# Optimization experiments

Hardware: AMD Instinct MI355X
Metric: run time of the kernel (lower is better)

Reference implementation:

```python
import jax, jax.numpy as jnp
import numpy as np

B, S, D = 2, 2048, 1024
N_HEADS = 16
HEAD_DIM = D // N_HEADS  # 64, even for RoPE
THETA = 10000.0


def rope_tables(seq, head_dim, dtype=jnp.float32):
    half = head_dim // 2
    freqs = 1.0 / (THETA ** (jnp.arange(half, dtype=jnp.float32) / half))
    angles = jnp.arange(seq, dtype=jnp.float32)[:, None] * freqs[None, :]  # [S, half]
    return jnp.cos(angles).astype(dtype), jnp.sin(angles).astype(dtype)


def apply_rope_interleaved(x, cos, sin):
    # x: [b, h, s, d]; even/odd interleaving
    x_even = x[..., 0::2]
    x_odd = x[..., 1::2]
    r_even = x_even * cos - x_odd * sin
    r_odd = x_even * sin + x_odd * cos
    # interleave back: stack on last axis then reshape
    out = jnp.stack([r_even, r_odd], axis=-1).reshape(x.shape)
    return out


def setup_inputs() -> dict:
    key = jax.random.key(0)
    ks = jax.random.split(key, 6)
    scale = 1.0 / np.sqrt(D)
    return {
        "x": jax.random.normal(ks[0], (B, S, D), dtype=jnp.float32),
        "Wq": jax.random.normal(ks[1], (D, D), dtype=jnp.float32) * scale,
        "Wk": jax.random.normal(ks[2], (D, D), dtype=jnp.float32) * scale,
        "Wv": jax.random.normal(ks[3], (D, D), dtype=jnp.float32) * scale,
        "Wo": jax.random.normal(ks[4], (D, D), dtype=jnp.float32) * scale,
        "bo": jnp.zeros((D,), dtype=jnp.float32),
    }


def reference(x, Wq, Wk, Wv, Wo, bo):
    b, s, _ = x.shape
    # QKV projections (no bias), split heads -> [b, h, s, hd]
    def proj(W):
        return jnp.einsum('bsd,de->bse', x, W).reshape(b, s, N_HEADS, HEAD_DIM).transpose(0, 2, 1, 3)
    q, k, v = proj(Wq), proj(Wk), proj(Wv)

    cos, sin = rope_tables(s, HEAD_DIM, x.dtype)  # [s, hd//2]
    q = apply_rope_interleaved(q, cos, sin)
    k = apply_rope_interleaved(k, cos, sin)

    scale = 1.0 / jnp.sqrt(jnp.asarray(HEAD_DIM, dtype=x.dtype))
    scores = jnp.einsum('bhqd,bhkd->bhqk', q, k) * scale  # [b, h, s, s]
    causal = jnp.tril(jnp.ones((s, s), dtype=bool))
    scores = jnp.where(causal[None, None], scores, jnp.asarray(-jnp.inf, dtype=scores.dtype))
    attn = jax.nn.softmax(scores, axis=-1)
    ctx = jnp.einsum('bhqk,bhkd->bhqd', attn, v)  # [b, h, s, hd]
    ctx = ctx.transpose(0, 2, 1, 3).reshape(b, s, N_HEADS * HEAD_DIM)
    return jnp.einsum('bsd,de->bse', ctx, Wo) + bo
```

## Files before the change

### kernel.cpp

```cpp
#include <hip/hip_runtime.h>
#include <hip/hip_bf16.h>
#include <math.h>

constexpr int Bb   = 2;
constexpr int S    = 2048;
constexpr int D    = 1024;
constexpr int H    = 16;
constexpr int Dh   = 64;
constexpr int HALF = 32;
constexpr int M    = Bb * S;
constexpr int K    = 1024;
constexpr int N    = 1024;

typedef __attribute__((ext_vector_type(8))) short short8;
typedef __attribute__((ext_vector_type(4))) float f32x4;

__device__ __forceinline__ unsigned short f2bf(float f) {
    unsigned int u = __float_as_uint(f);
    unsigned int r = (u + 0x7fffu + ((u >> 16) & 1u)) >> 16;
    return (unsigned short)r;
}

__device__ __forceinline__ void gl_lds16(const unsigned short* g, unsigned short* lds_base) {
    __builtin_amdgcn_global_load_lds(
        (const __attribute__((address_space(1))) unsigned int*)g,
        (__attribute__((address_space(3))) unsigned int*)lds_base, 16, 0, 0);
}

__global__ __launch_bounds__(256) void prep_kernel(
    const float* __restrict__ x,
    const float* W0, const float* W1, const float* W2, const float* W3,
    unsigned short* __restrict__ xb,
    unsigned short* T0, unsigned short* T1, unsigned short* T2, unsigned short* T3,
    float* __restrict__ cosT, float* __restrict__ sinT)
{
    __shared__ float tile[64][65];
    const int bid = blockIdx.x;
    const int tid = threadIdx.x;

    if (bid < 256) {
        int idx = bid * 256 + tid;
        int s = idx >> 5;
        int i = idx & 31;
        double freq = exp(-(double)i * (log(10000.0) / 32.0));
        double ang  = (double)s * freq;
        cosT[idx] = (float)cos(ang);
        sinT[idx] = (float)sin(ang);
    } else if (bid < 256 + 4096) {
        size_t i = (size_t)(bid - 256) * 256 + tid;
        float4 v = *(const float4*)(x + i * 4);
        ushort4 pk;
        pk.x = f2bf(v.x); pk.y = f2bf(v.y); pk.z = f2bf(v.z); pk.w = f2bf(v.w);
        *(ushort4*)(xb + i * 4) = pk;
    } else {
        int wb = bid - 4352;
        int z  = wb >> 8;
        int rem = wb & 255;
        const float* W = (z == 0) ? W0 : (z == 1) ? W1 : (z == 2) ? W2 : W3;
        unsigned short* T = (z == 0) ? T0 : (z == 1) ? T1 : (z == 2) ? T2 : T3;
        const int bk = (rem >> 4) * 64;
        const int bn = (rem & 15) * 64;
        const int lr = tid >> 4;
        const int lc = (tid & 15) * 4;

        #pragma unroll
        for (int i = 0; i < 4; ++i) {
            int r = lr + i * 16;
            float4 v = *(const float4*)(W + (size_t)(bk + r) * N + bn + lc);
            tile[r][lc + 0] = v.x; tile[r][lc + 1] = v.y;
            tile[r][lc + 2] = v.z; tile[r][lc + 3] = v.w;
        }
        __syncthreads();
        #pragma unroll
        for (int i = 0; i < 4; ++i) {
            int nr = lr + i * 16;
            ushort4 pk;
            pk.x = f2bf(tile[lc + 0][nr]);
            pk.y = f2bf(tile[lc + 1][nr]);
            pk.z = f2bf(tile[lc + 2][nr]);
            pk.w = f2bf(tile[lc + 3][nr]);
            *(ushort4*)(T + (size_t)(bn + nr) * K + bk + lc) = pk;
        }
    }
}

__global__ __launch_bounds__(512, 2) void gemm_qkv_kernel(
    const unsigned short* __restrict__ A,
    const unsigned short* __restrict__ BT,
    unsigned short* outQ, unsigned short* outK, unsigned short* outV,
    const float* __restrict__ cosT, const float* __restrict__ sinT)
{
    constexpr int NT    = 16;
    constexpr int ASLOT = 256 * 64;
    constexpr int BSLOT = 192 * 64;
    __shared__ __align__(16) unsigned short As[2 * ASLOT];
    __shared__ __align__(16) unsigned short Bs[2 * BSLOT];

    const int tid  = threadIdx.x;
    const int wid  = tid >> 6;
    const int lane = tid & 63;
    const int col  = lane & 15;
    const int quad = lane >> 4;
    const int wr   = wid >> 2;
    const int wc   = wid & 3;

    const int mbase = blockIdx.y * 256;
    const int nbase = blockIdx.x * 192;

    const int srow8 = lane >> 3;
    const int sch8  = lane & 7;
    const unsigned short *pA[4], *pB[3];
    unsigned short *dA[4], *dB[3];
    #pragma unroll
    for (int w = 0; w < 4; ++w) {
        int r = wid * 32 + w * 8 + srow8;
        pA[w] = A + (size_t)(mbase + r) * K + ((sch8 + (r >> 1)) & 7) * 8;
        dA[w] = &As[(wid * 32 + w * 8) * 64];
    }
    #pragma unroll
    for (int w = 0; w < 3; ++w) {
        int r = wid * 24 + w * 8 + srow8;
        pB[w] = BT + (size_t)(nbase + r) * K + ((sch8 + (r >> 1)) & 7) * 8;
        dB[w] = &Bs[(wid * 24 + w * 8) * 64];
    }

    int aoff[2][8], boff[2][3];
    #pragma unroll
    for (int kh = 0; kh < 2; ++kh) {
        #pragma unroll
        for (int f = 0; f < 8; ++f) {
            int r = wr * 128 + f * 16 + col;
            aoff[kh][f] = r * 64 + (((kh * 4 + quad) - (r >> 1)) & 7) * 8;
        }
        #pragma unroll
        for (int n = 0; n < 3; ++n) {
            int r = wc * 48 + n * 16 + col;
            boff[kh][n] = r * 64 + (((kh * 4 + quad) - (r >> 1)) & 7) * 8;
        }
    }

    f32x4 acc[8][3];
    #pragma unroll
    for (int f = 0; f < 8; ++f)
        #pragma unroll
        for (int n = 0; n < 3; ++n) acc[f][n] = (f32x4)0.f;

    auto stageA = [&](int slot) {
        #pragma unroll
        for (int w = 0; w < 4; ++w) { gl_lds16(pA[w], dA[w] + slot * ASLOT); pA[w] += 64; }
    };
    auto stageB = [&](int slot) {
        #pragma unroll
        for (int w = 0; w < 3; ++w) { gl_lds16(pB[w], dB[w] + slot * BSLOT); pB[w] += 64; }
    };

    stageA(0); stageB(0);
    asm volatile("s_waitcnt vmcnt(0)" ::: "memory");
    __builtin_amdgcn_s_barrier();
    __builtin_amdgcn_sched_barrier(0);

    #pragma unroll 1
    for (int t = 0; t < NT; ++t) {
        const unsigned short* Ab = &As[(t & 1) * ASLOT];
        const unsigned short* Bc = &Bs[(t & 1) * BSLOT];
        const int ns = (t + 1) & 1;
        short8 af[4], bf[3];

        #pragma unroll
        for (int i = 0; i < 4; ++i) af[i] = *(const short8*)&Ab[aoff[0][i]];
        #pragma unroll
        for (int n = 0; n < 3; ++n) bf[n] = *(const short8*)&Bc[boff[0][n]];
        if (t < NT - 1) stageA(ns);
        __builtin_amdgcn_sched_barrier(0);
        __builtin_amdgcn_s_barrier();
        asm volatile("s_waitcnt lgkmcnt(0)" ::: "memory");
        __builtin_amdgcn_s_setprio(1);
        #pragma unroll
        for (int i = 0; i < 4; ++i)
            #pragma unroll
            for (int n = 0; n < 3; ++n)
                acc[i][n] = __builtin_amdgcn_mfma_f32_16x16x32_bf16(af[i], bf[n], acc[i][n], 0, 0, 0);
        __builtin_amdgcn_s_setprio(0);
        __builtin_amdgcn_sched_barrier(0);
        __builtin_amdgcn_s_barrier();
        __builtin_amdgcn_sched_barrier(0);

        #pragma unroll
        for (int i = 0; i < 4; ++i) af[i] = *(const short8*)&Ab[aoff[0][4 + i]];
        if (t < NT - 1) stageB(ns);
        __builtin_amdgcn_sched_barrier(0);
        __builtin_amdgcn_s_barrier();
        asm volatile("s_waitcnt lgkmcnt(0)" ::: "memory");
        __builtin_amdgcn_s_setprio(1);
        #pragma unroll
        for (int i = 0; i < 4; ++i)
            #pragma unroll
            for (int n = 0; n < 3; ++n)
                acc[4 + i][n] = __builtin_amdgcn_mfma_f32_16x16x32_bf16(af[i], bf[n], acc[4 + i][n], 0, 0, 0);
        __builtin_amdgcn_s_setprio(0);
        __builtin_amdgcn_sched_barrier(0);
        __builtin_amdgcn_s_barrier();
        __builtin_amdgcn_sched_barrier(0);

        #pragma unroll
        for (int i = 0; i < 4; ++i) af[i] = *(const short8*)&Ab[aoff[1][i]];
        #pragma unroll
        for (int n = 0; n < 3; ++n) bf[n] = *(const short8*)&Bc[boff[1][n]];
        __builtin_amdgcn_sched_barrier(0);
        __builtin_amdgcn_s_barrier();
        asm volatile("s_waitcnt lgkmcnt(0)" ::: "memory");
        __builtin_amdgcn_s_setprio(1);
        #pragma unroll
        for (int i = 0; i < 4; ++i)
            #pragma unroll
            for (int n = 0; n < 3; ++n)
                acc[i][n] = __builtin_amdgcn_mfma_f32_16x16x32_bf16(af[i], bf[n], acc[i][n], 0, 0, 0);
        __builtin_amdgcn_s_setprio(0);
        __builtin_amdgcn_sched_barrier(0);
        __builtin_amdgcn_s_barrier();
        __builtin_amdgcn_sched_barrier(0);

        #pragma unroll
        for (int i = 0; i < 4; ++i) af[i] = *(const short8*)&Ab[aoff[1][4 + i]];
        __builtin_amdgcn_sched_barrier(0);
        __builtin_amdgcn_s_barrier();
        asm volatile("s_waitcnt lgkmcnt(0)" ::: "memory");
        __builtin_amdgcn_s_setprio(1);
        #pragma unroll
        for (int i = 0; i < 4; ++i)
            #pragma unroll
            for (int n = 0; n < 3; ++n)
                acc[4 + i][n] = __builtin_amdgcn_mfma_f32_16x16x32_bf16(af[i], bf[n], acc[4 + i][n], 0, 0, 0);
        __builtin_amdgcn_s_setprio(0);
        if (t < NT - 1) { asm volatile("s_waitcnt vmcnt(0)" ::: "memory"); }
        __builtin_amdgcn_sched_barrier(0);
        __builtin_amdgcn_s_barrier();
        __builtin_amdgcn_sched_barrier(0);
    }

    #pragma unroll
    for (int n = 0; n < 3; ++n) {
        int n_g = nbase + wc * 48 + n * 16 + col;
        int z   = n_g >> 10;
        int nl  = n_g & 1023;
        int h = nl >> 6, dh0 = nl & 63;
        if (z < 2) {
            unsigned short* o = z ? outK : outQ;
            int p = dh0 >> 1;
            bool even = !(dh0 & 1);
            #pragma unroll
            for (int f = 0; f < 8; ++f)
                #pragma unroll
                for (int reg = 0; reg < 4; ++reg) {
                    int m_g = mbase + wr * 128 + f * 16 + quad * 4 + reg;
                    int b = m_g >> 11, s = m_g & 2047;
                    float v = acc[f][n][reg];
                    float part = __shfl_xor(v, 1, 64);
                    float c = cosT[s * HALF + p], sn = sinT[s * HALF + p];
                    float r = even ? (v * c - part * sn) : (v * c + part * sn);
                    o[((size_t)(b * H + h) * S + s) * Dh + dh0] = f2bf(r);
                }
        } else {
            #pragma unroll
            for (int f = 0; f < 8; ++f) {
                int m0 = mbase + wr * 128 + f * 16 + quad * 4;
                int b = m0 >> 11, s = m0 & 2047;
                ushort4 pk;
                pk.x = f2bf(acc[f][n][0]);
                pk.y = f2bf(acc[f][n][1]);
                pk.z = f2bf(acc[f][n][2]);
                pk.w = f2bf(acc[f][n][3]);
                *(ushort4*)&outV[((size_t)(b * H + h) * Dh + dh0) * S + s] = pk;
            }
        }
    }
}

__global__ __launch_bounds__(256) void gemm_out_kernel(
    const unsigned short* __restrict__ A,
    const unsigned short* __restrict__ BT,
    float* __restrict__ outO, const float* __restrict__ bias)
{
    constexpr int BK   = 64;
    constexpr int ABUF = 64 * BK;
    constexpr int BBUF = 64 * BK;
    __shared__ __align__(16) unsigned short As[2 * ABUF];
    __shared__ __align__(16) unsigned short Bs[2 * BBUF];

    const int tid  = threadIdx.x;
    const int wave = tid >> 6;
    const int lane = tid & 63;
    const int col  = lane & 15;
    const int quad = lane >> 4;
    const int wy   = wave >> 1;
    const int wx   = wave & 1;

    const int mbase = blockIdx.y * 64;
    const int nbase = blockIdx.x * 64;

    const int srow8 = lane >> 3;
    const int sch8  = lane & 7;

    const unsigned short *pA[2], *pB[2];
    unsigned short *dA[2], *dB[2];
    #pragma unroll
    for (int w = 0; w < 2; ++w) {
        int base = wave * 16 + w * 8;
        int tr = base + srow8;
        pA[w] = A  + (size_t)(mbase + tr) * K + ((sch8 + (tr >> 1)) & 7) * 8;
        pB[w] = BT + (size_t)(nbase + tr) * K + ((sch8 + (tr >> 1)) & 7) * 8;
        dA[w] = &As[base * BK];
        dB[w] = &Bs[base * BK];
    }

    int aoff[2][2], boff[2][2];
    #pragma unroll
    for (int ks = 0; ks < 2; ++ks) {
        #pragma unroll
        for (int mi = 0; mi < 2; ++mi) {
            int r = wy * 32 + mi * 16 + col;
            aoff[ks][mi] = r * BK + (((ks * 4 + quad) - (r >> 1)) & 7) * 8;
        }
        #pragma unroll
        for (int ni = 0; ni < 2; ++ni) {
            int r = wx * 32 + ni * 16 + col;
            boff[ks][ni] = r * BK + (((ks * 4 + quad) - (r >> 1)) & 7) * 8;
        }
    }

    f32x4 acc[2][2];
    #pragma unroll
    for (int mi = 0; mi < 2; ++mi)
        #pragma unroll
        for (int ni = 0; ni < 2; ++ni) acc[mi][ni] = (f32x4)0.f;

    auto stage = [&](int buf) {
        #pragma unroll
        for (int w = 0; w < 2; ++w) { gl_lds16(pA[w], dA[w] + buf * ABUF); pA[w] += BK; }
        #pragma unroll
        for (int w = 0; w < 2; ++w) { gl_lds16(pB[w], dB[w] + buf * BBUF); pB[w] += BK; }
    };
    auto compute = [&](int buf) {
        const unsigned short* Ac = &As[buf * ABUF];
        const unsigned short* Bc = &Bs[buf * BBUF];
        #pragma unroll
        for (int ks = 0; ks < 2; ++ks) {
            short8 af[2], bfr[2];
            #pragma unroll
            for (int mi = 0; mi < 2; ++mi) af[mi] = *(const short8*)&Ac[aoff[ks][mi]];
            #pragma unroll
            for (int ni = 0; ni < 2; ++ni) bfr[ni] = *(const short8*)&Bc[boff[ks][ni]];
            #pragma unroll
            for (int mi = 0; mi < 2; ++mi)
                #pragma unroll
                for (int ni = 0; ni < 2; ++ni)
                    acc[mi][ni] = __builtin_amdgcn_mfma_f32_16x16x32_bf16(af[mi], bfr[ni], acc[mi][ni], 0, 0, 0);
        }
    };

    stage(0);
    #pragma unroll 1
    for (int kk = 0; kk < 16; kk += 2) {
        __syncthreads();
        if (kk + 1 < 16) stage(1);
        compute(0);
        __syncthreads();
        if (kk + 2 < 16) stage(0);
        compute(1);
    }

    #pragma unroll
    for (int ni = 0; ni < 2; ++ni) {
        int n_g = nbase + wx * 32 + ni * 16 + col;
        float bv = bias[n_g];
        #pragma unroll
        for (int mi = 0; mi < 2; ++mi)
            #pragma unroll
            for (int reg = 0; reg < 4; ++reg) {
                int m_g = mbase + wy * 32 + mi * 16 + quad * 4 + reg;
                outO[(size_t)m_g * N + n_g] = acc[mi][ni][reg] + bv;
            }
    }
}

__global__ __launch_bounds__(256) void attn_mfma_kernel(
    const unsigned short* __restrict__ q, const unsigned short* __restrict__ k,
    const unsigned short* __restrict__ vt,
    float* __restrict__ Opart, float* __restrict__ lpart)
{
    constexpr int TSZ = 64 * 64;
    __shared__ __align__(16) unsigned short Ks[2 * TSZ];
    __shared__ __align__(16) unsigned short Vs[2 * TSZ];
    __shared__ __align__(16) unsigned short Ps[4][16 * 64];

    const int tid  = threadIdx.x;
    const int wave = tid >> 6;
    const int lane = tid & 63;
    const int col  = lane & 15;
    const int quad = lane >> 4;
    const int l8   = lane >> 3, cp = lane & 7;

    const int pairh = blockIdx.x;
    const int pair  = pairh >> 1;
    const int hpar  = pairh & 1;
    const int bh = blockIdx.y;
    const unsigned short* qb = q  + (size_t)bh * S * Dh;
    const unsigned short* kb = k  + (size_t)bh * S * Dh;
    const unsigned short* vb = vt + (size_t)bh * Dh * S;

    unsigned short* dk0 = &Ks[(wave * 16 + 0) * 64];
    unsigned short* dk1 = &Ks[(wave * 16 + 8) * 64];
    unsigned short* dv0 = &Vs[(wave * 16 + 0) * 64];
    unsigned short* dv1 = &Vs[(wave * 16 + 8) * 64];

    int foff[2][4];
    #pragma unroll
    for (int ks = 0; ks < 2; ++ks)
        #pragma unroll
        for (int nt = 0; nt < 4; ++nt) {
            int r = nt * 16 + col;
            foff[ks][nt] = r * 64 + (((ks * 4 + quad) - r) & 7) * 8;
        }
    int poffW[4][4];
    #pragma unroll
    for (int nt = 0; nt < 4; ++nt)
        #pragma unroll
        for (int reg = 0; reg < 4; ++reg) {
            int row = quad * 4 + reg;
            poffW[nt][reg] = row * 64 + (((nt * 2 + (col >> 3)) ^ (row & 7)) << 3) + (col & 7);
        }
    int poffR[2];
    #pragma unroll
    for (int ks = 0; ks < 2; ++ks)
        poffR[ks] = col * 64 + (((ks * 4 + quad) ^ (col & 7)) << 3);

    for (int phase = 0; phase < 2; ++phase) {
        const int qt  = phase ? (31 - pair) : pair;
        const int wr0 = qt * 64 + wave * 16;

        const unsigned short *pk0, *pk1, *pv0, *pv1;
        {
            int r0 = wave * 16 + l8, r1 = r0 + 8;
            pk0 = kb + (size_t)(hpar * 64 + r0) * Dh + ((cp + r0) & 7) * 8;
            pk1 = kb + (size_t)(hpar * 64 + r1) * Dh + ((cp + r1) & 7) * 8;
            pv0 = vb + (size_t)r0 * S + hpar * 64 + ((cp + r0) & 7) * 8;
            pv1 = vb + (size_t)r1 * S + hpar * 64 + ((cp + r1) & 7) * 8;
        }

        auto stageKV = [&](int buf) {
            gl_lds16(pk0, dk0 + buf * TSZ); gl_lds16(pk1, dk1 + buf * TSZ);
            gl_lds16(pv0, dv0 + buf * TSZ); gl_lds16(pv1, dv1 + buf * TSZ);
            pk0 += 128 * Dh; pk1 += 128 * Dh; pv0 += 128; pv1 += 128;
        };

        __syncthreads();
        if (hpar <= qt) stageKV(0);

        short8 qfrag[2];
        #pragma unroll
        for (int ks = 0; ks < 2; ++ks)
            qfrag[ks] = *(const short8*)(qb + (size_t)(wr0 + col) * Dh + ks * 32 + quad * 8);

        f32x4 O[4];
        float lacc[4];
        #pragma unroll
        for (int nt = 0; nt < 4; ++nt) O[nt] = (f32x4)0.f;
        #pragma unroll
        for (int r = 0; r < 4; ++r) lacc[r] = 0.f;

        auto subtile = [&](const unsigned short* Kc, const unsigned short* Vc, int t) {
            f32x4 sacc[4];
            #pragma unroll
            for (int nt = 0; nt < 4; ++nt) sacc[nt] = (f32x4)0.f;
            #pragma unroll
            for (int ks = 0; ks < 2; ++ks)
                #pragma unroll
                for (int nt = 0; nt < 4; ++nt) {
                    short8 kf = *(const short8*)&Kc[foff[ks][nt]];
                    sacc[nt] = __builtin_amdgcn_mfma_f32_16x16x32_bf16(qfrag[ks], kf, sacc[nt], 0, 0, 0);
                }
            float pb[4][4];
            #pragma unroll
            for (int nt = 0; nt < 4; ++nt) {
                int key_l = nt * 16 + col;
                #pragma unroll
                for (int reg = 0; reg < 4; ++reg) {
                    float e = __builtin_amdgcn_exp2f(
                        fmaf(sacc[nt][reg], 0.18033688011112042f, -11.541560327111707f));
                    if (t == qt && key_l > wave * 16 + quad * 4 + reg) e = 0.f;
                    pb[nt][reg] = e;
                }
            }
            #pragma unroll
            for (int reg = 0; reg < 4; ++reg)
                lacc[reg] += (pb[0][reg] + pb[1][reg]) + (pb[2][reg] + pb[3][reg]);
            #pragma unroll
            for (int nt = 0; nt < 4; ++nt)
                #pragma unroll
                for (int reg = 0; reg < 4; ++reg)
                    Ps[wave][poffW[nt][reg]] = f2bf(pb[nt][reg]);
            #pragma unroll
            for (int ks = 0; ks < 2; ++ks) {
                short8 pf = *(const short8*)&Ps[wave][poffR[ks]];
                #pragma unroll
                for (int nt = 0; nt < 4; ++nt) {
                    short8 vf = *(const short8*)&Vc[foff[ks][nt]];
                    O[nt] = __builtin_amdgcn_mfma_f32_16x16x32_bf16(pf, vf, O[nt], 0, 0, 0);
                }
            }
        };

        int j = 0;
        for (int i = hpar; i <= qt; i += 2, ++j) {
            __syncthreads();
            if (i + 2 <= qt) stageKV((j + 1) & 1);
            subtile(&Ks[(j & 1) * TSZ], &Vs[(j & 1) * TSZ], i);
        }

        #pragma unroll
        for (int reg = 0; reg < 4; ++reg) {
            float s = lacc[reg];
            #pragma unroll
            for (int off = 1; off <= 8; off <<= 1)
                s += __shfl_xor(s, off, 64);
            lacc[reg] = s;
        }

        const size_t pb_base = (size_t)(hpar * 32 + bh) * S;
        #pragma unroll
        for (int reg = 0; reg < 4; ++reg) {
            int rg = wr0 + quad * 4 + reg;
            float* op = Opart + (pb_base + rg) * 64 + col;
            #pragma unroll
            for (int nt = 0; nt < 4; ++nt)
                op[nt * 16] = O[nt][reg];
            if (col == 0)
                lpart[pb_base + rg] = lacc[reg];
        }
    }
}

__global__ __launch_bounds__(256) void combine_kernel(
    const float* __restrict__ Opart, const float* __restrict__ lpart,
    unsigned short* __restrict__ ctx)
{
    int gid = blockIdx.x * 256 + threadIdx.x;
    int bh  = gid >> 15;
    int rem = gid & 32767;
    int qr  = rem >> 4;
    int dg  = (rem & 15) << 2;

    size_t i0 = ((size_t)bh * S + qr) * 64 + dg;
    size_t i1 = ((size_t)(32 + bh) * S + qr) * 64 + dg;
    float4 a = *(const float4*)(Opart + i0);
    float4 c = *(const float4*)(Opart + i1);
    float inv = 1.0f / (lpart[(size_t)bh * S + qr] + lpart[(size_t)(32 + bh) * S + qr]);

    int b = bh >> 4, hh = bh & 15;
    ushort4 pk;
    pk.x = f2bf((a.x + c.x) * inv);
    pk.y = f2bf((a.y + c.y) * inv);
    pk.z = f2bf((a.z + c.z) * inv);
    pk.w = f2bf((a.w + c.w) * inv);
    *(ushort4*)(ctx + ((size_t)b * S + qr) * 1024 + hh * 64 + dg) = pk;
}

extern "C" void kernel_launch(void* const* d_in, const int* in_sizes, int n_in,
                              void* d_out, int out_size, void* d_ws, size_t ws_size,
                              hipStream_t stream) {
    const float* x  = (const float*)d_in[0];
    const float* Wq = (const float*)d_in[1];
    const float* Wk = (const float*)d_in[2];
    const float* Wv = (const float*)d_in[3];
    const float* Wo = (const float*)d_in[4];
    const float* bo = (const float*)d_in[5];
    float* out = (float*)d_out;

    const size_t MK  = (size_t)M * K;
    const size_t NK  = (size_t)N * K;
    const size_t QKV = (size_t)Bb * H * S * Dh;

    unsigned short* xb   = (unsigned short*)d_ws;
    unsigned short* WqT  = xb  + MK;
    unsigned short* WkT  = WqT + NK;
    unsigned short* WvT  = WkT + NK;
    unsigned short* WoT  = WvT + NK;
    unsigned short* qbuf = WoT + NK;
    unsigned short* kbuf = qbuf + QKV;
    unsigned short* vtb  = kbuf + QKV;
    unsigned short* ctxb = vtb  + QKV;
    float* cosT  = (float*)(ctxb + QKV);
    float* sinT  = cosT + (size_t)S * HALF;
    float* Opart = sinT + (size_t)S * HALF;
    float* lpart = Opart + (size_t)2 * 32 * S * 64;

    prep_kernel<<<5376, 256, 0, stream>>>(x, Wq, Wk, Wv, Wo,
                                          xb, WqT, WkT, WvT, WoT, cosT, sinT);

    gemm_qkv_kernel<<<dim3(16, 16), 512, 0, stream>>>(
        xb, WqT, qbuf, kbuf, vtb, cosT, sinT);

    attn_mfma_kernel<<<dim3(32, Bb * H), 256, 0, stream>>>(qbuf, kbuf, vtb, Opart, lpart);

    combine_kernel<<<4096, 256, 0, stream>>>(Opart, lpart, ctxb);

    gemm_out_kernel<<<dim3(16, 64), 256, 0, stream>>>(ctxb, WoT, out, bo);
}
```

Measured before the change: 190.0 us.

## Grow attention query tile to 128 rows with 8 waves sharing K/V staging

The attention kernel now uses 512-thread blocks of 8 waves covering 128 query rows, which halves the grid and the number of K/V tiles each block stages. Each wave stages a single 8-row slice of K and V per tile and skips key tiles that lie entirely above its diagonal. Causal masking now uses global key indices and is applied only on edge tiles. The intent is better K/V reuse per LDS load and fewer redundant global loads. In exchange there are more idle waves near the diagonal, since every wave waits at each barrier, and fewer blocks to spread across CUs.

```diff
diff --git a/kernel.cpp b/kernel.cpp
--- a/kernel.cpp
+++ b/kernel.cpp
@@ -383,7 +383,7 @@
     }
 }
 
-__global__ __launch_bounds__(256) void attn_mfma_kernel(
+__global__ __launch_bounds__(512, 4) void attn_mfma_kernel(
     const unsigned short* __restrict__ q, const unsigned short* __restrict__ k,
     const unsigned short* __restrict__ vt,
     float* __restrict__ Opart, float* __restrict__ lpart)
@@ -391,14 +391,14 @@
     constexpr int TSZ = 64 * 64;
     __shared__ __align__(16) unsigned short Ks[2 * TSZ];
     __shared__ __align__(16) unsigned short Vs[2 * TSZ];
-    __shared__ __align__(16) unsigned short Ps[4][16 * 64];
+    __shared__ __align__(16) unsigned short Ps[8][16 * 64];
 
     const int tid  = threadIdx.x;
     const int wave = tid >> 6;
     const int lane = tid & 63;
     const int col  = lane & 15;
     const int quad = lane >> 4;
-    const int l8   = lane >> 3, cp = lane & 7;
+    const int r8   = lane >> 3, cp = lane & 7;
 
     const int pairh = blockIdx.x;
     const int pair  = pairh >> 1;
@@ -408,10 +408,8 @@
     const unsigned short* kb = k  + (size_t)bh * S * Dh;
     const unsigned short* vb = vt + (size_t)bh * Dh * S;
 
-    unsigned short* dk0 = &Ks[(wave * 16 + 0) * 64];
-    unsigned short* dk1 = &Ks[(wave * 16 + 8) * 64];
-    unsigned short* dv0 = &Vs[(wave * 16 + 0) * 64];
-    unsigned short* dv1 = &Vs[(wave * 16 + 8) * 64];
+    unsigned short* dk = &Ks[(wave * 8) * 64];
+    unsigned short* dv = &Vs[(wave * 8) * 64];
 
     int foff[2][4];
     #pragma unroll
@@ -435,26 +433,25 @@
         poffR[ks] = col * 64 + (((ks * 4 + quad) ^ (col & 7)) << 3);
 
     for (int phase = 0; phase < 2; ++phase) {
-        const int qt  = phase ? (31 - pair) : pair;
-        const int wr0 = qt * 64 + wave * 16;
-
-        const unsigned short *pk0, *pk1, *pv0, *pv1;
+        const int qt  = phase ? (15 - pair) : pair;
+        const int wr0 = qt * 128 + wave * 16;
+        const int NV  = qt + 1;
+
+        const unsigned short *pk, *pv;
         {
-            int r0 = wave * 16 + l8, r1 = r0 + 8;
-            pk0 = kb + (size_t)(hpar * 64 + r0) * Dh + ((cp + r0) & 7) * 8;
-            pk1 = kb + (size_t)(hpar * 64 + r1) * Dh + ((cp + r1) & 7) * 8;
-            pv0 = vb + (size_t)r0 * S + hpar * 64 + ((cp + r0) & 7) * 8;
-            pv1 = vb + (size_t)r1 * S + hpar * 64 + ((cp + r1) & 7) * 8;
-        }
-
+            int r = wave * 8 + r8;
+            pk = kb + (size_t)(hpar * 64 + r) * Dh + ((cp + r) & 7) * 8;
+            pv = vb + (size_t)r * S + hpar * 64 + ((cp + r) & 7) * 8;
+        }
         auto stageKV = [&](int buf) {
-            gl_lds16(pk0, dk0 + buf * TSZ); gl_lds16(pk1, dk1 + buf * TSZ);
-            gl_lds16(pv0, dv0 + buf * TSZ); gl_lds16(pv1, dv1 + buf * TSZ);
-            pk0 += 128 * Dh; pk1 += 128 * Dh; pv0 += 128; pv1 += 128;
+            gl_lds16(pk, dk + buf * TSZ);
+            gl_lds16(pv, dv + buf * TSZ);
+            pk += 128 * Dh;
+            pv += 128;
         };
 
         __syncthreads();
-        if (hpar <= qt) stageKV(0);
+        stageKV(0);
 
         short8 qfrag[2];
         #pragma unroll
@@ -479,15 +476,16 @@
                     short8 kf = *(const short8*)&Kc[foff[ks][nt]];
                     sacc[nt] = __builtin_amdgcn_mfma_f32_16x16x32_bf16(qfrag[ks], kf, sacc[nt], 0, 0, 0);
                 }
+            const bool edge = (t * 64 + 63 > wr0);
             float pb[4][4];
             #pragma unroll
             for (int nt = 0; nt < 4; ++nt) {
-                int key_l = nt * 16 + col;
+                int key_g = t * 64 + nt * 16 + col;
                 #pragma unroll
                 for (int reg = 0; reg < 4; ++reg) {
                     float e = __builtin_amdgcn_exp2f(
                         fmaf(sacc[nt][reg], 0.18033688011112042f, -11.541560327111707f));
-                    if (t == qt && key_l > wave * 16 + quad * 4 + reg) e = 0.f;
+                    if (edge && key_g > wr0 + quad * 4 + reg) e = 0.f;
                     pb[nt][reg] = e;
                 }
             }
@@ -510,11 +508,12 @@
             }
         };
 
-        int j = 0;
-        for (int i = hpar; i <= qt; i += 2, ++j) {
+        for (int j = 0; j < NV; ++j) {
             __syncthreads();
-            if (i + 2 <= qt) stageKV((j + 1) & 1);
-            subtile(&Ks[(j & 1) * TSZ], &Vs[(j & 1) * TSZ], i);
+            if (j + 1 < NV) stageKV((j + 1) & 1);
+            const int t = hpar + 2 * j;
+            if (t * 64 <= wr0 + 15)
+                subtile(&Ks[(j & 1) * TSZ], &Vs[(j & 1) * TSZ], t);
         }
 
         #pragma unroll
@@ -600,7 +599,7 @@
     gemm_qkv_kernel<<<dim3(16, 16), 512, 0, stream>>>(
         xb, WqT, qbuf, kbuf, vtb, cosT, sinT);
 
-    attn_mfma_kernel<<<dim3(32, Bb * H), 256, 0, stream>>>(qbuf, kbuf, vtb, Opart, lpart);
+    attn_mfma_kernel<<<dim3(16, Bb * H), 512, 0, stream>>>(qbuf, kbuf, vtb, Opart, lpart);
 
     combine_kernel<<<4096, 256, 0, stream>>>(Opart, lpart, ctxb);
 
```

Result: no change. 189.9 us (-0.1%).
